# Performance work log

Measured on AMD Instinct MI355X. Metric: run time of the kernel, lower is better.

Reference implementation:

```python
import jax, jax.numpy as jnp
import numpy as np

B, F, T, C, H, HH = 16384, 2048, 64, 32, 24, 48  # batch, features, n_tails, cluster_size, tail_hidden, head_hidden


def setup_inputs() -> dict:
    key = jax.random.key(0)
    ks = jax.random.split(key, 8)
    x = jax.random.normal(ks[0], (B, F), dtype=jnp.float32)
    clusters = jnp.arange(T * C, dtype=jnp.int32).reshape(T, C)  # equal-size partition of features
    # tied autoencoder weights: encoder = x @ W + hb, decoder = h @ W.T + vb
    Wt = jax.random.normal(ks[1], (T, C, H), dtype=jnp.float32) * 0.1
    hb = jax.random.normal(ks[2], (T, H), dtype=jnp.float32) * 0.1
    vb = jax.random.normal(ks[3], (T, C), dtype=jnp.float32) * 0.1
    Wh = jax.random.normal(ks[4], (T, HH), dtype=jnp.float32) * 0.1
    hbh = jax.random.normal(ks[5], (HH,), dtype=jnp.float32) * 0.1
    vbh = jax.random.normal(ks[6], (T,), dtype=jnp.float32) * 0.1
    return {"x": x, "clusters": clusters, "Wt": Wt, "hb": hb, "vb": vb,
            "Wh": Wh, "hbh": hbh, "vbh": vbh}


def reference(x, clusters, Wt, hb, vb, Wh, hbh, vbh):
    # gather all clusters in one shot: [B, T, C]
    xg = x[:, clusters]
    # batched tiny autoencoders (encode then decode with tied weight W)
    h = jnp.einsum('btc,tch->bth', xg, Wt) + hb[None, :, :]
    out = jnp.einsum('bth,tch->btc', h, Wt) + vb[None, :, :]
    # per-tail log-RMSE over (batch, cluster) elements -> [T]
    rmse = jnp.sqrt(jnp.mean(jnp.square(out - xg), axis=(0, 2)))
    tails = jnp.log(rmse)
    # head autoencoder on the tail-loss vector
    hh = tails @ Wh + hbh          # [HH]
    head_out = hh @ Wh.T + vbh     # [T]
    return head_out, tails
```

## Files before the change

kernel.cpp:

```cpp
#include <hip/hip_runtime.h>
#include <cstddef>

#define B_  16384
#define F_  2048
#define T_  64
#define C_  32
#define H_  24
#define HH_ 48
#define ROWS 256
#define PAD  33

__global__ __launch_bounds__(256) void kitnet_main(
    const float* __restrict__ x, const int* __restrict__ clusters,
    const float* __restrict__ Wt, const float* __restrict__ hb,
    const float* __restrict__ vb, float* __restrict__ sse)
{
    __shared__ __align__(16) float WtL[C_ * H_];
    __shared__ float xgL[ROWS * PAD];
    __shared__ float hbL[H_];
    __shared__ float vbL[C_];
    __shared__ int   colsL[C_];
    __shared__ int   contigF;
    __shared__ float wsum[4];

    const int tid = threadIdx.x;
    const int t  = blockIdx.x & (T_ - 1);
    const int b0 = (blockIdx.x >> 6) * ROWS;

    if (tid < C_) colsL[tid] = clusters[t * C_ + tid];
    for (int i = tid; i < C_ * H_; i += 256) WtL[i] = Wt[t * C_ * H_ + i];
    if (tid < H_) hbL[tid] = hb[t * H_ + tid];
    if (tid < C_) vbL[tid] = vb[t * C_ + tid];
    __syncthreads();
    if (tid == 0) {
        int ok = (colsL[0] & 3) == 0;
        for (int c = 1; c < C_; ++c) ok &= (colsL[c] == colsL[0] + c);
        contigF = ok;
    }
    __syncthreads();

    if (contigF) {
        const int col0 = colsL[0];
        #pragma unroll
        for (int p = 0; p < 8; ++p) {
            const int idx = p * 256 + tid;
            const int row = idx >> 3, c4 = idx & 7;
            const float4 v = *(const float4*)(x + (size_t)(b0 + row) * F_ + col0 + c4 * 4);
            float* dst = &xgL[row * PAD + c4 * 4];
            dst[0] = v.x; dst[1] = v.y; dst[2] = v.z; dst[3] = v.w;
        }
    } else {
        #pragma unroll
        for (int p = 0; p < 32; ++p) {
            const int idx = p * 256 + tid;
            const int row = idx >> 5, c = idx & 31;
            xgL[row * PAD + c] = x[(size_t)(b0 + row) * F_ + colsL[c]];
        }
    }
    __syncthreads();

    float xv[C_];
    #pragma unroll
    for (int c = 0; c < C_; ++c) xv[c] = xgL[tid * PAD + c];

    float h[H_];
    #pragma unroll
    for (int j = 0; j < H_; ++j) h[j] = hbL[j];

    #pragma unroll 4
    for (int c = 0; c < C_; ++c) {
        const float xc = xv[c];
        const float4* wr = (const float4*)&WtL[c * H_];
        #pragma unroll
        for (int j4 = 0; j4 < 6; ++j4) {
            const float4 w = wr[j4];
            h[j4 * 4 + 0] += xc * w.x;
            h[j4 * 4 + 1] += xc * w.y;
            h[j4 * 4 + 2] += xc * w.z;
            h[j4 * 4 + 3] += xc * w.w;
        }
    }

    float err = 0.f;
    #pragma unroll 4
    for (int c = 0; c < C_; ++c) {
        const float4* wr = (const float4*)&WtL[c * H_];
        float acc = vbL[c];
        #pragma unroll
        for (int j4 = 0; j4 < 6; ++j4) {
            const float4 w = wr[j4];
            acc += h[j4 * 4 + 0] * w.x + h[j4 * 4 + 1] * w.y
                 + h[j4 * 4 + 2] * w.z + h[j4 * 4 + 3] * w.w;
        }
        const float d = acc - xv[c];
        err += d * d;
    }

    #pragma unroll
    for (int off = 32; off > 0; off >>= 1) err += __shfl_down(err, off, 64);
    if ((tid & 63) == 0) wsum[tid >> 6] = err;
    __syncthreads();
    if (tid == 0) atomicAdd(&sse[t], wsum[0] + wsum[1] + wsum[2] + wsum[3]);
}

__global__ __launch_bounds__(64) void kitnet_head(
    const float* __restrict__ sse, const float* __restrict__ Wh,
    const float* __restrict__ hbh, const float* __restrict__ vbh,
    float* __restrict__ out)
{
    __shared__ float tl[T_];
    __shared__ float hhL[HH_];
    const int tid = threadIdx.x;

    const float tail = 0.5f * logf(sse[tid] * (1.0f / ((float)B_ * (float)C_)));
    tl[tid] = tail;
    out[T_ + tid] = tail;
    __syncthreads();

    if (tid < HH_) {
        float acc = hbh[tid];
        #pragma unroll 8
        for (int t = 0; t < T_; ++t) acc += tl[t] * Wh[t * HH_ + tid];
        hhL[tid] = acc;
    }
    __syncthreads();

    float ho = vbh[tid];
    #pragma unroll 8
    for (int j = 0; j < HH_; ++j) ho += hhL[j] * Wh[tid * HH_ + j];
    out[tid] = ho;
}

extern "C" void kernel_launch(void* const* d_in, const int* in_sizes, int n_in,
                              void* d_out, int out_size, void* d_ws, size_t ws_size,
                              hipStream_t stream)
{
    const float* x        = (const float*)d_in[0];
    const int*   clusters = (const int*)  d_in[1];
    const float* Wt       = (const float*)d_in[2];
    const float* hb       = (const float*)d_in[3];
    const float* vb       = (const float*)d_in[4];
    const float* Wh       = (const float*)d_in[5];
    const float* hbh      = (const float*)d_in[6];
    const float* vbh      = (const float*)d_in[7];
    float* out = (float*)d_out;
    float* sse = (float*)d_ws;

    hipMemsetAsync(sse, 0, T_ * sizeof(float), stream);
    kitnet_main<<<dim3(T_ * (B_ / ROWS)), dim3(256), 0, stream>>>(x, clusters, Wt, hb, vb, sse);
    kitnet_head<<<dim3(1), dim3(64), 0, stream>>>(sse, Wh, hbh, vbh, out);
}
```

Baseline: 243.5 us.

## Load x rows directly into registers and read weights via scalar loads

Drops the shared-memory staging of the gathered x tile and the weights. Each thread now reads its own 32-float row slice straight from global memory as float4s, and reads Wt, hb and vb directly from global memory, which are wave-uniform and can be served by scalar loads. The contiguity check becomes a wave ballot, and the compute loops are fully unrolled. This removes LDS traffic and two barriers. In exchange, each thread's 128-byte row read is uncoalesced across the wave, and register pressure rises from full unrolling.

```diff
diff --git a/kernel.cpp b/kernel.cpp
--- a/kernel.cpp
+++ b/kernel.cpp
@@ -8,90 +8,58 @@
 #define H_  24
 #define HH_ 48
 #define ROWS 256
-#define PAD  33
 
 __global__ __launch_bounds__(256) void kitnet_main(
     const float* __restrict__ x, const int* __restrict__ clusters,
     const float* __restrict__ Wt, const float* __restrict__ hb,
     const float* __restrict__ vb, float* __restrict__ sse)
 {
-    __shared__ __align__(16) float WtL[C_ * H_];
-    __shared__ float xgL[ROWS * PAD];
-    __shared__ float hbL[H_];
-    __shared__ float vbL[C_];
-    __shared__ int   colsL[C_];
-    __shared__ int   contigF;
     __shared__ float wsum[4];
 
     const int tid = threadIdx.x;
-    const int t  = blockIdx.x & (T_ - 1);
-    const int b0 = (blockIdx.x >> 6) * ROWS;
+    const int t   = blockIdx.x & (T_ - 1);
+    const int b   = (blockIdx.x >> 6) * ROWS + tid;
 
-    if (tid < C_) colsL[tid] = clusters[t * C_ + tid];
-    for (int i = tid; i < C_ * H_; i += 256) WtL[i] = Wt[t * C_ * H_ + i];
-    if (tid < H_) hbL[tid] = hb[t * H_ + tid];
-    if (tid < C_) vbL[tid] = vb[t * C_ + tid];
-    __syncthreads();
-    if (tid == 0) {
-        int ok = (colsL[0] & 3) == 0;
-        for (int c = 1; c < C_; ++c) ok &= (colsL[c] == colsL[0] + c);
-        contigF = ok;
-    }
-    __syncthreads();
+    const float* wt = Wt + t * (C_ * H_);
+    const int*   cl = clusters + t * C_;
 
-    if (contigF) {
-        const int col0 = colsL[0];
+    const int col0 = cl[0];
+    const int myc  = cl[tid & (C_ - 1)];
+    const bool okl = (myc == col0 + (tid & (C_ - 1)));
+    const bool contig = (__ballot(okl) == ~0ULL) && ((col0 & 3) == 0);
+
+    float xv[C_];
+    if (contig) {
+        const float4* xr = (const float4*)(x + (size_t)b * F_ + col0);
         #pragma unroll
-        for (int p = 0; p < 8; ++p) {
-            const int idx = p * 256 + tid;
-            const int row = idx >> 3, c4 = idx & 7;
-            const float4 v = *(const float4*)(x + (size_t)(b0 + row) * F_ + col0 + c4 * 4);
-            float* dst = &xgL[row * PAD + c4 * 4];
-            dst[0] = v.x; dst[1] = v.y; dst[2] = v.z; dst[3] = v.w;
+        for (int q = 0; q < C_ / 4; ++q) {
+            const float4 v = xr[q];
+            xv[q * 4 + 0] = v.x; xv[q * 4 + 1] = v.y;
+            xv[q * 4 + 2] = v.z; xv[q * 4 + 3] = v.w;
         }
     } else {
+        const float* xrow = x + (size_t)b * F_;
         #pragma unroll
-        for (int p = 0; p < 32; ++p) {
-            const int idx = p * 256 + tid;
-            const int row = idx >> 5, c = idx & 31;
-            xgL[row * PAD + c] = x[(size_t)(b0 + row) * F_ + colsL[c]];
-        }
+        for (int c = 0; c < C_; ++c) xv[c] = xrow[cl[c]];
     }
-    __syncthreads();
-
-    float xv[C_];
-    #pragma unroll
-    for (int c = 0; c < C_; ++c) xv[c] = xgL[tid * PAD + c];
 
     float h[H_];
     #pragma unroll
-    for (int j = 0; j < H_; ++j) h[j] = hbL[j];
+    for (int j = 0; j < H_; ++j) h[j] = hb[t * H_ + j];
 
-    #pragma unroll 4
+    #pragma unroll
     for (int c = 0; c < C_; ++c) {
         const float xc = xv[c];
-        const float4* wr = (const float4*)&WtL[c * H_];
         #pragma unroll
-        for (int j4 = 0; j4 < 6; ++j4) {
-            const float4 w = wr[j4];
-            h[j4 * 4 + 0] += xc * w.x;
-            h[j4 * 4 + 1] += xc * w.y;
-            h[j4 * 4 + 2] += xc * w.z;
-            h[j4 * 4 + 3] += xc * w.w;
-        }
+        for (int j = 0; j < H_; ++j) h[j] += wt[c * H_ + j] * xc;
     }
 
     float err = 0.f;
-    #pragma unroll 4
+    #pragma unroll
     for (int c = 0; c < C_; ++c) {
-        const float4* wr = (const float4*)&WtL[c * H_];
-        float acc = vbL[c];
+        float acc = vb[t * C_ + c];
         #pragma unroll
-        for (int j4 = 0; j4 < 6; ++j4) {
-            const float4 w = wr[j4];
-            acc += h[j4 * 4 + 0] * w.x + h[j4 * 4 + 1] * w.y
-                 + h[j4 * 4 + 2] * w.z + h[j4 * 4 + 3] * w.w;
-        }
+        for (int j = 0; j < H_; ++j) acc += h[j] * wt[c * H_ + j];
         const float d = acc - xv[c];
         err += d * d;
     }
```

New measurement: 275.8 us. 1.13x slower.
